# Performance work log

Hardware: AMD Instinct MI355X
Metric: run time of the kernel (lower is better)

## Reference

```python
import jax, jax.numpy as jnp
import numpy as np

D_MODEL = 2048
D_STATE = 128
D_CONV = 4
EXPAND = 2
HEADDIM = 64
NGROUPS = 1
D_INNER = EXPAND * D_MODEL            # 4096
NHEADS = D_INNER // HEADDIM           # 64
D_XBC = D_INNER + 2 * NGROUPS * D_STATE   # 4352
D_IN_PROJ = 2 * D_INNER + 2 * NGROUPS * D_STATE + NHEADS  # 8512
BLOCK_LEN = 64


def _segsum(x):
    # x: (..., T) -> (..., T, T) with segsum[i, j] = sum_{j < k <= i} x[k], -inf above diag
    T = x.shape[-1]
    xc = jnp.cumsum(x, axis=-1)
    seg = xc[..., :, None] - xc[..., None, :]
    mask = jnp.tril(jnp.ones((T, T), dtype=bool))
    return jnp.where(mask, seg, -jnp.inf)


def _ssd_scan(X, A, B, C, block_len):
    # X: (b, L, h, p), A: (b, L, h), B/C: (b, L, h, n)
    b, L, h, p = X.shape
    c = L // block_len
    X = X.reshape(b, c, block_len, h, p)
    A = A.reshape(b, c, block_len, h).transpose(0, 3, 1, 2)  # b h c l
    B = B.reshape(b, c, block_len, h, -1)
    C = C.reshape(b, c, block_len, h, -1)
    A_cumsum = jnp.cumsum(A, axis=-1)                         # b h c l
    Lmat = jnp.exp(_segsum(A))                                # b h c l l
    Y_diag = jnp.einsum('bclhn,bcshn,bhcls,bcshp->bclhp', C, B, Lmat, X)
    decay_states = jnp.exp(A_cumsum[:, :, :, -1:] - A_cumsum)  # b h c l
    states = jnp.einsum('bclhn,bhcl,bclhp->bchpn', B, decay_states, X)
    init = jnp.zeros_like(states[:, :1])
    states = jnp.concatenate([init, states], axis=1)          # b (c+1) h p n
    A_last = jnp.pad(A_cumsum[:, :, :, -1], ((0, 0), (0, 0), (1, 0)))  # b h (c+1)
    decay_chunk = jnp.exp(_segsum(A_last))                    # b h (c+1) (c+1)
    new_states = jnp.einsum('bhzc,bchpn->bzhpn', decay_chunk, states)
    states = new_states[:, 1:]                                # b c h p n
    state_decay_out = jnp.exp(A_cumsum)                       # b h c l
    Y_off = jnp.einsum('bclhn,bchpn,bhcl->bclhp', C, states, state_decay_out)
    return (Y_diag + Y_off).reshape(b, L, h, p)


def _forward(x, in_proj_w, conv_w, conv_b, A_log, D, dt_bias, norm_w, out_proj_w):
    Bsz, L, _ = x.shape
    proj = x @ in_proj_w.T                                    # (B, L, d_in_proj)
    z = proj[:, :, :D_INNER]
    xBC = proj[:, :, D_INNER:D_INNER + D_XBC]
    dt_raw = proj[:, :, D_INNER + D_XBC:]
    # depthwise causal conv1d (torch pads both sides then truncates to L == left pad only)
    xBC_t = xBC.transpose(0, 2, 1)                            # (B, C, L)
    conv = jax.lax.conv_general_dilated(
        xBC_t, conv_w, window_strides=(1,), padding=[(D_CONV - 1, 0)],
        feature_group_count=D_XBC, dimension_numbers=('NCH', 'OIH', 'NCH'))
    conv = conv + conv_b[None, :, None]
    xBC = jax.nn.silu(conv).transpose(0, 2, 1)                # (B, L, d_xBC)
    x_ssm = xBC[:, :, :D_INNER]
    B_param = xBC[:, :, D_INNER:D_INNER + NGROUPS * D_STATE]
    C_param = xBC[:, :, D_INNER + NGROUPS * D_STATE:]
    dt = jax.nn.softplus(dt_raw + dt_bias)                    # (B, L, nheads)
    A = -jnp.exp(A_log)                                       # (nheads,)
    x_heads = x_ssm.reshape(Bsz, L, NHEADS, HEADDIM)
    hpg = NHEADS // NGROUPS
    X = x_heads * dt[..., None]
    A_disc = dt * A[None, None, :]
    B_heads = jnp.repeat(B_param.reshape(Bsz, L, NGROUPS, D_STATE), hpg, axis=2)
    C_heads = jnp.repeat(C_param.reshape(Bsz, L, NGROUPS, D_STATE), hpg, axis=2)
    pad_len = (BLOCK_LEN - L % BLOCK_LEN) % BLOCK_LEN
    if pad_len > 0:
        X = jnp.pad(X, ((0, 0), (0, pad_len), (0, 0), (0, 0)))
        A_disc = jnp.pad(A_disc, ((0, 0), (0, pad_len), (0, 0)))
        B_heads = jnp.pad(B_heads, ((0, 0), (0, pad_len), (0, 0), (0, 0)))
        C_heads = jnp.pad(C_heads, ((0, 0), (0, pad_len), (0, 0), (0, 0)))
    Y = _ssd_scan(X, A_disc, B_heads, C_heads, BLOCK_LEN)[:, :L]
    Y = Y + x_heads * D[None, None, :, None]
    y = Y.reshape(Bsz, L, D_INNER)
    y = y * jax.nn.silu(z)
    rms = jnp.sqrt(jnp.mean(y * y, axis=-1, keepdims=True) + 1e-5)
    y = y / rms * norm_w
    return y @ out_proj_w.T


def setup_inputs() -> dict:
    key = jax.random.key(0)
    ks = jax.random.split(key, 8)
    x = jax.random.normal(ks[0], (2, 2048, D_MODEL), dtype=jnp.float32)
    in_proj_w = jax.random.normal(ks[1], (D_IN_PROJ, D_MODEL), dtype=jnp.float32) * 0.02
    conv_w = jax.random.normal(ks[2], (D_XBC, 1, D_CONV), dtype=jnp.float32) * 0.2
    conv_b = jnp.zeros((D_XBC,), dtype=jnp.float32)
    A_log = jnp.log(jnp.arange(1, NHEADS + 1, dtype=jnp.float32))
    D = jnp.ones((NHEADS,), dtype=jnp.float32)
    dt_bias = jax.random.normal(ks[3], (NHEADS,), dtype=jnp.float32) * 0.1
    norm_w = jnp.ones((D_INNER,), dtype=jnp.float32)
    out_proj_w = jax.random.normal(ks[4], (D_MODEL, D_INNER), dtype=jnp.float32) * 0.02
    return {"x": x, "in_proj_w": in_proj_w, "conv_w": conv_w, "conv_b": conv_b,
            "A_log": A_log, "D": D, "dt_bias": dt_bias, "norm_w": norm_w,
            "out_proj_w": out_proj_w}


def reference(x, in_proj_w, conv_w, conv_b, A_log, D, dt_bias, norm_w, out_proj_w):
    return _forward(x, in_proj_w, conv_w, conv_b, A_log, D, dt_bias, norm_w, out_proj_w)
```

## Files before the change

### kernel.cpp

```cpp
#include <hip/hip_runtime.h>
#include <cstddef>
#include <cstdint>

#define B_SZ    2
#define SEQ     2048
#define DMODEL  2048
#define DINNER  4096
#define DSTATE  128
#define NHEADS  64
#define HEADDIM 64
#define DXBC    4352
#define NPROJ   8448
#define CHUNK   64
#define NCHUNK  32
#define TOKENS  (B_SZ*SEQ)

typedef __attribute__((ext_vector_type(8))) short short8;
typedef __attribute__((ext_vector_type(4))) float floatx4;

__device__ inline float us2f(unsigned short u) {
  union { uint32_t i; float f; } c; c.i = ((uint32_t)u) << 16; return c.f;
}
__device__ inline unsigned short f2us(float f) {
  union { float f; uint32_t i; } c; c.f = f;
  uint32_t r = (c.i + 0x7fffu + ((c.i >> 16) & 1u)) >> 16;
  return (unsigned short)r;
}
__device__ inline float plo(uint32_t v) {
  union { uint32_t i; float f; } c; c.i = v << 16; return c.f;
}
__device__ inline float phi(uint32_t v) {
  union { uint32_t i; float f; } c; c.i = v & 0xffff0000u; return c.f;
}

__global__ __launch_bounds__(256) void cast_f32_bf16(
    const float* __restrict__ src, unsigned short* __restrict__ dst, int n) {
  int i = (blockIdx.x * 256 + threadIdx.x) * 4;
  if (i < n) {
    float4 v = *(const float4*)(src + i);
    ushort4 o;
    o.x = f2us(v.x); o.y = f2us(v.y); o.z = f2us(v.z); o.w = f2us(v.w);
    *(ushort4*)(dst + i) = o;
  }
}

template<int OUT_BF16>
__global__ __launch_bounds__(256, 2) void gemm_bt_p3(
    const unsigned short* __restrict__ A, const unsigned short* __restrict__ B,
    void* __restrict__ Cout, int M, int N, int K, int GM) {
  __shared__ __align__(16) unsigned short sT[3 * 12288];
  const int tid  = threadIdx.x;
  const int lane = tid & 63;
  const int wc   = tid >> 6;
  const int fr   = lane & 15;
  const int fq   = lane >> 4;

  const int nwg  = gridDim.x;
  int wgid = blockIdx.x;
  if ((nwg & 7) == 0) wgid = (wgid & 7) * (nwg >> 3) + (wgid >> 3);
  const int bm = (wgid % GM) * 128;
  const int bn = (wgid / GM) * 256;

  floatx4 acc[8][4];
  #pragma unroll
  for (int i = 0; i < 8; ++i)
    #pragma unroll
    for (int j = 0; j < 4; ++j) acc[i][j] = (floatx4){0.f, 0.f, 0.f, 0.f};

  auto stage = [&](int rb, int kb) {
    unsigned short* dst = (unsigned short*)sT + rb * 12288;
    #pragma unroll
    for (int q = 0; q < 6; ++q) {
      if (q < 2) {
        int i = q * 256 + tid;
        int row = i >> 2, slot = i & 3;
        const unsigned short* g =
            A + (size_t)(bm + row) * K + kb + 8 * (slot ^ ((row >> 1) & 3));
        __builtin_amdgcn_global_load_lds(
            (const __attribute__((address_space(1))) uint32_t*)g,
            (__attribute__((address_space(3))) uint32_t*)(dst + i * 8), 16, 0, 0);
      } else {
        int i = (q - 2) * 256 + tid;
        int row = i >> 2, slot = i & 3;
        const unsigned short* g =
            B + (size_t)(bn + row) * K + kb + 8 * (slot ^ ((row >> 1) & 3));
        __builtin_amdgcn_global_load_lds(
            (const __attribute__((address_space(1))) uint32_t*)g,
            (__attribute__((address_space(3))) uint32_t*)(dst + 4096 + i * 8), 16, 0, 0);
      }
    }
  };

  const int NH = K >> 5;
  stage(0, 0);
  stage(1, 32);
  asm volatile("s_waitcnt vmcnt(6)" ::: "memory");
  asm volatile("s_barrier" ::: "memory");

  int cb = 0, sb = 2;
  for (int h = 0; h < NH; ++h) {
    const unsigned short* buf = (const unsigned short*)sT + cb * 12288;
    if (h + 2 < NH) stage(sb, (h + 2) << 5);

    short8 af[8], bf[4];
    #pragma unroll
    for (int i = 0; i < 8; ++i) {
      int row = i * 16 + fr;
      af[i] = *(const short8*)(buf + row * 32 + 8 * (fq ^ ((row >> 1) & 3)));
    }
    #pragma unroll
    for (int j = 0; j < 4; ++j) {
      int row = wc * 64 + j * 16 + fr;
      bf[j] = *(const short8*)(buf + 4096 + row * 32 + 8 * (fq ^ ((row >> 1) & 3)));
    }
    __builtin_amdgcn_s_setprio(1);
    #pragma unroll
    for (int i = 0; i < 8; ++i)
      #pragma unroll
      for (int j = 0; j < 4; ++j)
        acc[i][j] = __builtin_amdgcn_mfma_f32_16x16x32_bf16(af[i], bf[j], acc[i][j], 0, 0, 0);
    __builtin_amdgcn_s_setprio(0);

    if (h < NH - 2) asm volatile("s_waitcnt vmcnt(6) lgkmcnt(0)" ::: "memory");
    else            asm volatile("s_waitcnt vmcnt(0) lgkmcnt(0)" ::: "memory");
    asm volatile("s_barrier" ::: "memory");
    cb = (cb == 2) ? 0 : cb + 1;
    sb = (sb == 2) ? 0 : sb + 1;
  }

  #pragma unroll
  for (int i = 0; i < 8; ++i) {
    #pragma unroll
    for (int j = 0; j < 4; ++j) {
      int col = bn + wc * 64 + j * 16 + fr;
      #pragma unroll
      for (int r = 0; r < 4; ++r) {
        int row = bm + i * 16 + fq * 4 + r;
        if (OUT_BF16)
          ((unsigned short*)Cout)[(size_t)row * N + col] = f2us(acc[i][j][r]);
        else
          ((float*)Cout)[(size_t)row * N + col] = acc[i][j][r];
      }
    }
  }
}

__device__ inline void loadA4(const float* p, float* d) {
  float4 v = *(const float4*)p; d[0]=v.x; d[1]=v.y; d[2]=v.z; d[3]=v.w;
}
__device__ inline void loadA4(const unsigned short* p, float* d) {
  ushort4 v = *(const ushort4*)p;
  d[0]=us2f(v.x); d[1]=us2f(v.y); d[2]=us2f(v.z); d[3]=us2f(v.w);
}
__device__ inline void store8(float* C, size_t off, const float* v) {
  *(float4*)(C + off)     = make_float4(v[0], v[1], v[2], v[3]);
  *(float4*)(C + off + 4) = make_float4(v[4], v[5], v[6], v[7]);
}
__device__ inline void store8(unsigned short* C, size_t off, const float* v) {
  ushort4 a; a.x=f2us(v[0]); a.y=f2us(v[1]); a.z=f2us(v[2]); a.w=f2us(v[3]);
  ushort4 b; b.x=f2us(v[4]); b.y=f2us(v[5]); b.z=f2us(v[6]); b.w=f2us(v[7]);
  *(ushort4*)(C + off) = a; *(ushort4*)(C + off + 4) = b;
}

template<typename AT, typename OT>
__global__ __launch_bounds__(256) void gemm_nt(
    const AT* __restrict__ A, const float* __restrict__ Bw,
    OT* __restrict__ C, int M, int N, int K) {
  __shared__ float As[16][128+4];
  __shared__ float Bs[16][128+4];
  const int bm = blockIdx.y * 128;
  const int bn = blockIdx.x * 128;
  const int tid = threadIdx.x;
  const int tx = tid & 15, ty = tid >> 4;

  float acc[8][8];
  #pragma unroll
  for (int i = 0; i < 8; ++i)
    #pragma unroll
    for (int j = 0; j < 8; ++j) acc[i][j] = 0.f;

  for (int k0 = 0; k0 < K; k0 += 16) {
    #pragma unroll
    for (int r = 0; r < 2; ++r) {
      int i = tid + r * 256;
      int m  = i >> 2;
      int kv = (i & 3) << 2;
      float va[4];
      loadA4(A + (size_t)(bm + m) * K + k0 + kv, va);
      As[kv+0][m] = va[0]; As[kv+1][m] = va[1]; As[kv+2][m] = va[2]; As[kv+3][m] = va[3];
      float vb[4] = {0.f, 0.f, 0.f, 0.f};
      if (bn + m < N) loadA4(Bw + (size_t)(bn + m) * K + k0 + kv, vb);
      Bs[kv+0][m] = vb[0]; Bs[kv+1][m] = vb[1]; Bs[kv+2][m] = vb[2]; Bs[kv+3][m] = vb[3];
    }
    __syncthreads();
    #pragma unroll
    for (int kk = 0; kk < 16; ++kk) {
      float ra[8], rb[8];
      *(float4*)&ra[0] = *(const float4*)&As[kk][ty*8];
      *(float4*)&ra[4] = *(const float4*)&As[kk][ty*8+4];
      *(float4*)&rb[0] = *(const float4*)&Bs[kk][tx*8];
      *(float4*)&rb[4] = *(const float4*)&Bs[kk][tx*8+4];
      #pragma unroll
      for (int i = 0; i < 8; ++i)
        #pragma unroll
        for (int j = 0; j < 8; ++j) acc[i][j] += ra[i] * rb[j];
    }
    __syncthreads();
  }
  #pragma unroll
  for (int i = 0; i < 8; ++i) {
    int m  = bm + ty*8 + i;
    int n0 = bn + tx*8;
    if (n0 < N) store8(C, (size_t)m * N + n0, &acc[i][0]);
  }
}

__global__ __launch_bounds__(256) void dt_gemm(
    const float* __restrict__ x, const float* __restrict__ W,
    float* __restrict__ dtr) {
  __shared__ float sX[32][64];
  __shared__ float sW[32][64];
  const int tid = threadIdx.x;
  const int t0 = blockIdx.x * 64;
  const int tx = tid & 15;
  const int ty = tid >> 4;
  const float* Wdt = W + (size_t)NPROJ * DMODEL;

  float acc[4][4];
  #pragma unroll
  for (int i = 0; i < 4; ++i)
    #pragma unroll
    for (int j = 0; j < 4; ++j) acc[i][j] = 0.f;

  const int r  = tid >> 3;
  const int kq = (tid & 7) * 4;

  for (int k0 = 0; k0 < DMODEL; k0 += 32) {
    __syncthreads();
    #pragma unroll
    for (int rr = 0; rr < 2; ++rr) {
      int t = r + rr * 32;
      float4 v = *(const float4*)(x + (size_t)(t0 + t) * DMODEL + k0 + kq);
      sX[kq+0][t] = v.x; sX[kq+1][t] = v.y; sX[kq+2][t] = v.z; sX[kq+3][t] = v.w;
    }
    #pragma unroll
    for (int rr = 0; rr < 2; ++rr) {
      int hh = r + rr * 32;
      float4 v = *(const float4*)(Wdt + (size_t)hh * DMODEL + k0 + kq);
      sW[kq+0][hh] = v.x; sW[kq+1][hh] = v.y; sW[kq+2][hh] = v.z; sW[kq+3][hh] = v.w;
    }
    __syncthreads();
    #pragma unroll
    for (int kk = 0; kk < 32; ++kk) {
      float4 ra = *(const float4*)&sX[kk][ty*4];
      float4 rb = *(const float4*)&sW[kk][tx*4];
      float a[4] = {ra.x, ra.y, ra.z, ra.w};
      float b[4] = {rb.x, rb.y, rb.z, rb.w};
      #pragma unroll
      for (int i = 0; i < 4; ++i)
        #pragma unroll
        for (int j = 0; j < 4; ++j)
          acc[i][j] += a[i] * b[j];
    }
  }
  #pragma unroll
  for (int i = 0; i < 4; ++i) {
    float4 o = make_float4(acc[i][0], acc[i][1], acc[i][2], acc[i][3]);
    *(float4*)(dtr + (size_t)(t0 + ty*4 + i) * NHEADS + tx*4) = o;
  }
}

__global__ __launch_bounds__(256) void bc_conv_g(
    const unsigned short* __restrict__ proj, const float* __restrict__ cw,
    const float* __restrict__ cb, unsigned short* __restrict__ bcact,
    float* __restrict__ gbuf) {
  const int c = blockIdx.x & 31;
  const int b = blockIdx.x >> 5;
  const int tid = threadIdx.x;
  const int t0 = b * SEQ + c * CHUNK;
  __shared__ unsigned short sB[64*130];
  __shared__ unsigned short sC[64*130];
  for (int i = tid; i < 64*256; i += 256) {
    int s = i >> 8, ch = i & 255;
    int cx = 4096 + ch;
    int lb = c * CHUNK + s;
    float acc = cb[cx];
    #pragma unroll
    for (int j = 0; j < 4; ++j) {
      int ll = lb - 3 + j;
      if (ll >= 0)
        acc += cw[cx*4 + j] * us2f(proj[(size_t)(b*SEQ + ll) * NPROJ + DINNER + cx]);
    }
    float v = acc / (1.f + expf(-acc));
    unsigned short uv = f2us(v);
    if (ch < 128) sB[s*130 + ch] = uv;
    else          sC[s*130 + (ch - 128)] = uv;
    bcact[(size_t)(t0 + s) * 256 + ch] = uv;
  }
  __syncthreads();
  const int l = tid >> 2, q = tid & 3;
  float g[16];
  #pragma unroll
  for (int j = 0; j < 16; ++j) g[j] = 0.f;
  const uint32_t* Cu = (const uint32_t*)&sC[l * 130];
  for (int u = 0; u < 64; ++u) {
    uint32_t cv = Cu[u];
    float c0 = plo(cv), c1 = phi(cv);
    #pragma unroll
    for (int j = 0; j < 16; ++j) {
      uint32_t bv = ((const uint32_t*)&sB[(q*16 + j) * 130])[u];
      g[j] += c0 * plo(bv) + c1 * phi(bv);
    }
  }
  float* gr = gbuf + ((size_t)(b*NCHUNK + c)) * 4096 + l*64 + q*16;
  #pragma unroll
  for (int j = 0; j < 16; ++j) gr[j] = g[j];
}

__global__ __launch_bounds__(256, 4) void ssd_phase_a2_mfma(
    const unsigned short* __restrict__ proj, const unsigned short* __restrict__ bcact,
    const float* __restrict__ dtr, const float* __restrict__ cw,
    const float* __restrict__ cb, const float* __restrict__ A_log,
    const float* __restrict__ dt_bias, const float* __restrict__ gbuf,
    const float* __restrict__ Dv,
    unsigned short* __restrict__ cs, float* __restrict__ acs,
    unsigned short* __restrict__ yscan) {
  const int h = blockIdx.x & 63;
  const int c = (blockIdx.x >> 6) & 31;
  const int b = blockIdx.x >> 11;
  const int tid = threadIdx.x;
  const int t0 = b * SEQ + c * CHUNK;
  const int lane = tid & 63, wave = tid >> 6;
  const int fr = lane & 15, fq = lane >> 4;

  __shared__ __align__(16) unsigned short sBt[128*72];
  __shared__ __align__(16) unsigned short sXh[64*72];
  __shared__ __align__(16) unsigned short sW[64*72];
  __shared__ float sdt[64], sAc[64], sdecay[64];

  const float Ah = -expf(A_log[h]);
  if (tid < 64) {
    float raw = dtr[(size_t)(t0 + tid) * NHEADS + h] + dt_bias[h];
    float dt = (raw > 20.f) ? raw : log1pf(expf(raw));
    sdt[tid] = dt;
    float v = dt * Ah;
    #pragma unroll
    for (int off = 1; off < 64; off <<= 1) {
      float o = __shfl_up(v, off, 64);
      if (tid >= off) v += o;
    }
    sAc[tid] = v;
    float alast = __shfl(v, 63, 64);
    sdecay[tid] = expf(alast - v);
    acs[((size_t)((b*NHEADS + h)*NCHUNK + c))*64 + tid] = v;
  }
  __syncthreads();
  for (int i = tid; i < 64*128; i += 256) {
    int s = i >> 7, n = i & 127;
    float v = us2f(bcact[(size_t)(t0 + s) * 256 + n]) * sdt[s] * sdecay[s];
    sBt[n*72 + s] = f2us(v);
  }
  for (int i = tid; i < 64*64; i += 256) {
    int s = i >> 6, p = i & 63;
    int cx = h * HEADDIM + p;
    int lb = c * CHUNK + s;
    float acc = cb[cx];
    #pragma unroll
    for (int j = 0; j < 4; ++j) {
      int ll = lb - 3 + j;
      if (ll >= 0)
        acc += cw[cx*4 + j] * us2f(proj[(size_t)(b*SEQ + ll) * NPROJ + DINNER + cx]);
    }
    float xh = acc / (1.f + expf(-acc));
    sXh[p*72 + s] = f2us(xh);
  }
  {
    const float* gr = gbuf + ((size_t)(b*NCHUNK + c)) * 4096;
    for (int i = tid; i < 4096; i += 256) {
      int l = i >> 6, s = i & 63;
      float w = (s <= l) ? gr[i] * expf(sAc[l] - sAc[s]) * sdt[s] : 0.f;
      sW[l*72 + s] = f2us(w);
    }
  }
  __syncthreads();

  floatx4 accy[4];
  #pragma unroll
  for (int j = 0; j < 4; ++j) accy[j] = (floatx4){0.f, 0.f, 0.f, 0.f};
  #pragma unroll
  for (int k0 = 0; k0 < 64; k0 += 32) {
    short8 af = *(const short8*)(sW + (wave*16 + fr)*72 + k0 + fq*8);
    #pragma unroll
    for (int j = 0; j < 4; ++j) {
      short8 bf = *(const short8*)(sXh + (j*16 + fr)*72 + k0 + fq*8);
      accy[j] = __builtin_amdgcn_mfma_f32_16x16x32_bf16(af, bf, accy[j], 0, 0, 0);
    }
  }
  const float Dh = Dv[h];
  #pragma unroll
  for (int j = 0; j < 4; ++j) {
    int p = j*16 + fr;
    #pragma unroll
    for (int r = 0; r < 4; ++r) {
      int l = wave*16 + fq*4 + r;
      float yd = accy[j][r] + us2f(sXh[p*72 + l]) * Dh;
      yscan[(size_t)(t0 + l) * DINNER + h*HEADDIM + p] = f2us(yd);
    }
  }
  floatx4 accs[8];
  #pragma unroll
  for (int j = 0; j < 8; ++j) accs[j] = (floatx4){0.f, 0.f, 0.f, 0.f};
  #pragma unroll
  for (int k0 = 0; k0 < 64; k0 += 32) {
    short8 af = *(const short8*)(sXh + (wave*16 + fr)*72 + k0 + fq*8);
    #pragma unroll
    for (int j = 0; j < 8; ++j) {
      short8 bf = *(const short8*)(sBt + (j*16 + fr)*72 + k0 + fq*8);
      accs[j] = __builtin_amdgcn_mfma_f32_16x16x32_bf16(af, bf, accs[j], 0, 0, 0);
    }
  }
  const size_t csb = ((size_t)((b*NHEADS + h)*NCHUNK + c)) * (HEADDIM*DSTATE);
  #pragma unroll
  for (int j = 0; j < 8; ++j) {
    int n = j*16 + fr;
    #pragma unroll
    for (int r = 0; r < 4; ++r) {
      int p = wave*16 + fq*4 + r;
      cs[csb + p*128 + n] = f2us(accs[j][r]);
    }
  }
}

__global__ __launch_bounds__(256) void ssd_scan_states(
    unsigned short* __restrict__ cs, const float* __restrict__ acs) {
  int idx = blockIdx.x * 256 + threadIdx.x;
  int e  = idx & 8191;
  int bh = idx >> 13;
  float S = 0.f;
  for (int c = 0; c < NCHUNK; ++c) {
    float al = acs[((size_t)bh*NCHUNK + c)*64 + 63];
    size_t o = ((size_t)bh*NCHUNK + c)*(HEADDIM*DSTATE) + e;
    S = S * expf(al) + us2f(cs[o]);
    cs[o] = f2us(S);
  }
}

__global__ __launch_bounds__(256, 4) void ssd_phase_c_mfma(
    const unsigned short* __restrict__ bcact, const unsigned short* __restrict__ cs,
    const float* __restrict__ acs, unsigned short* __restrict__ yscan) {
  const int h = blockIdx.x & 63;
  const int c = (blockIdx.x >> 6) & 31;
  const int b = blockIdx.x >> 11;
  const int tid = threadIdx.x;
  const int t0 = b * SEQ + c * CHUNK;
  const int lane = tid & 63, wave = tid >> 6;
  const int fr = lane & 15, fq = lane >> 4;

  __shared__ __align__(16) unsigned short sC[64*136];
  __shared__ __align__(16) unsigned short sS[64*136];
  __shared__ float seAc[64];

  const size_t csb = ((size_t)((b*NHEADS + h)*NCHUNK + c)) * (HEADDIM*DSTATE);
  for (int i = tid; i < 8192; i += 256) {
    int p = i >> 7, n = i & 127;
    sS[p*136 + n] = cs[csb + i];
  }
  for (int i = tid; i < 8192; i += 256) {
    int l = i >> 7, n = i & 127;
    sC[l*136 + n] = bcact[(size_t)(t0 + l) * 256 + 128 + n];
  }
  if (tid < 64) seAc[tid] = expf(acs[((size_t)((b*NHEADS + h)*NCHUNK + c))*64 + tid]);
  __syncthreads();

  floatx4 acc[4];
  #pragma unroll
  for (int j = 0; j < 4; ++j) acc[j] = (floatx4){0.f, 0.f, 0.f, 0.f};
  #pragma unroll
  for (int k0 = 0; k0 < 128; k0 += 32) {
    short8 af = *(const short8*)(sC + (wave*16 + fr)*136 + k0 + fq*8);
    #pragma unroll
    for (int j = 0; j < 4; ++j) {
      short8 bf = *(const short8*)(sS + (j*16 + fr)*136 + k0 + fq*8);
      acc[j] = __builtin_amdgcn_mfma_f32_16x16x32_bf16(af, bf, acc[j], 0, 0, 0);
    }
  }
  #pragma unroll
  for (int j = 0; j < 4; ++j) {
    int p = j*16 + fr;
    #pragma unroll
    for (int r = 0; r < 4; ++r) {
      int l = wave*16 + fq*4 + r;
      size_t yi = (size_t)(t0 + l) * DINNER + h*HEADDIM + p;
      yscan[yi] = f2us(us2f(yscan[yi]) + acc[j][r] * seAc[l]);
    }
  }
}

__global__ __launch_bounds__(256) void gate_rmsnorm2(
    const unsigned short* __restrict__ proj, const float* __restrict__ norm_w,
    unsigned short* __restrict__ yscan) {
  const int t = blockIdx.x;
  const int tid = threadIdx.x;
  __shared__ float ybuf[DINNER];
  __shared__ float wpart[4];
  __shared__ float sinv;
  float ss = 0.f;
  for (int i = tid; i < DINNER; i += 256) {
    float zv = us2f(proj[(size_t)t * NPROJ + i]);
    float yv = us2f(yscan[(size_t)t * DINNER + i]) * (zv / (1.f + expf(-zv)));
    ybuf[i] = yv;
    ss += yv * yv;
  }
  #pragma unroll
  for (int off = 32; off > 0; off >>= 1) ss += __shfl_down(ss, off, 64);
  if ((tid & 63) == 0) wpart[tid >> 6] = ss;
  __syncthreads();
  if (tid == 0) {
    float tot = wpart[0] + wpart[1] + wpart[2] + wpart[3];
    sinv = 1.f / sqrtf(tot / (float)DINNER + 1e-5f);
  }
  __syncthreads();
  float inv = sinv;
  for (int i = tid; i < DINNER; i += 256)
    yscan[(size_t)t * DINNER + i] = f2us(ybuf[i] * inv * norm_w[i]);
}

__global__ __launch_bounds__(512) void ssd_fused(
    const unsigned short* __restrict__ proj, const float* __restrict__ dtr,
    const float* __restrict__ cw, const float* __restrict__ cb,
    const float* __restrict__ A_log, const float* __restrict__ dt_bias,
    unsigned short* __restrict__ yscan) {
  const int h = blockIdx.x & 63;
  const int b = blockIdx.x >> 6;
  const int tid = threadIdx.x;

  __shared__ unsigned short sB[64*130];
  __shared__ unsigned short sC[64*130];
  __shared__ unsigned short sX[64*66];
  __shared__ float sW[64*65];
  __shared__ float sdt[64], sAc[64], sdecay[64], seAc[64];

  const float Ah = -expf(A_log[h]);
  const float dbias = dt_bias[h];

  float S[16];
  #pragma unroll
  for (int j = 0; j < 16; ++j) S[j] = 0.f;

  const int lG  = tid >> 3;
  const int oc  = tid & 7;

  for (int c = 0; c < NCHUNK; ++c) {
    const int t0 = b * SEQ + c * CHUNK;
    __syncthreads();
    if (tid < 64) {
      float raw = dtr[(size_t)(t0 + tid) * NHEADS + h] + dbias;
      sdt[tid] = (raw > 20.f) ? raw : log1pf(expf(raw));
    }
    for (int i = tid; i < 64*256; i += 512) {
      int s = i >> 8, ch = i & 255;
      int cx = 4096 + ch;
      int lb = c * CHUNK + s;
      float acc = cb[cx];
      #pragma unroll
      for (int j = 0; j < 4; ++j) {
        int ll = lb - 3 + j;
        if (ll >= 0)
          acc += cw[cx*4 + j] * us2f(proj[(size_t)(b*SEQ + ll) * NPROJ + DINNER + cx]);
      }
      float v = acc / (1.f + expf(-acc));
      if (ch < 128) sB[s*130 + ch] = f2us(v);
      else          sC[s*130 + (ch - 128)] = f2us(v);
    }
    __syncthreads();
    if (tid == 0) {
      float run = 0.f;
      for (int s = 0; s < CHUNK; ++s) { run += sdt[s] * Ah; sAc[s] = run; }
    }
    __syncthreads();
    if (tid < 64) {
      float last = sAc[63];
      sdecay[tid] = expf(last - sAc[tid]);
      seAc[tid]   = expf(sAc[tid]);
    }
    for (int i = tid; i < 64*64; i += 512) {
      int s = i >> 6, p = i & 63;
      int cx = h * HEADDIM + p;
      int lb = c * CHUNK + s;
      float acc = cb[cx];
      #pragma unroll
      for (int j = 0; j < 4; ++j) {
        int ll = lb - 3 + j;
        if (ll >= 0)
          acc += cw[cx*4 + j] * us2f(proj[(size_t)(b*SEQ + ll) * NPROJ + DINNER + cx]);
      }
      float v = acc / (1.f + expf(-acc));
      sX[s*66 + p] = f2us(v * sdt[s]);
    }
    __syncthreads();

    float g[8];
    #pragma unroll
    for (int j = 0; j < 8; ++j) g[j] = 0.f;
    {
      const uint32_t* Cu = (const uint32_t*)&sC[lG * 130];
      for (int u = 0; u < 64; ++u) {
        uint32_t cv = Cu[u];
        float c0 = plo(cv), c1 = phi(cv);
        #pragma unroll
        for (int j = 0; j < 8; ++j) {
          uint32_t bv = ((const uint32_t*)&sB[(oc*8 + j) * 130])[u];
          g[j] += c0 * plo(bv) + c1 * phi(bv);
        }
      }
    }
    {
      float acl = sAc[lG];
      #pragma unroll
      for (int j = 0; j < 8; ++j) {
        int s = oc*8 + j;
        sW[lG*65 + s] = (s <= lG) ? g[j] * expf(acl - sAc[s]) : 0.f;
      }
    }
    {
      float elast = expf(sAc[63]);
      #pragma unroll
      for (int j = 0; j < 16; ++j) S[j] *= elast;
      for (int s = 0; s < CHUNK; ++s) {
        float w = sdecay[s] * us2f(sX[s*66 + lG]);
        const uint32_t* Bu = (const uint32_t*)&sB[s*130 + oc*16];
        #pragma unroll
        for (int ju = 0; ju < 8; ++ju) {
          uint32_t bv = Bu[ju];
          S[2*ju]   += plo(bv) * w;
          S[2*ju+1] += phi(bv) * w;
        }
      }
    }
    __syncthreads();
    #pragma unroll
    for (int j = 0; j < 16; ++j) sB[lG*130 + oc*16 + j] = f2us(S[j]);
    __syncthreads();
    for (int o = tid; o < CHUNK*HEADDIM; o += 512) {
      int l = o >> 6, p = o & 63;
      float yd = 0.f;
      for (int s = 0; s <= l; ++s)
        yd += sW[l*65 + s] * us2f(sX[s*66 + p]);
      float yo = 0.f;
      const uint32_t* Cu = (const uint32_t*)&sC[l * 130];
      const uint32_t* Su = (const uint32_t*)&sB[p * 130];
      for (int u = 0; u < 64; ++u) {
        uint32_t cv = Cu[u], sv = Su[u];
        yo += plo(cv) * plo(sv) + phi(cv) * phi(sv);
      }
      float y = yd + yo * seAc[l];
      yscan[(size_t)(t0 + l) * DINNER + h * HEADDIM + p] = f2us(y);
    }
  }
}

__global__ __launch_bounds__(256) void gate_rmsnorm_dskip(
    const unsigned short* __restrict__ proj, const float* __restrict__ cw,
    const float* __restrict__ cb, const float* __restrict__ Dv,
    const float* __restrict__ norm_w, unsigned short* __restrict__ yscan) {
  const int t = blockIdx.x;
  const int tid = threadIdx.x;
  const int b = t >> 11, lb = t & 2047;
  __shared__ float ybuf[DINNER];
  __shared__ float wpart[4];
  __shared__ float sinv;
  float ss = 0.f;
  for (int i = tid; i < DINNER; i += 256) {
    float zv = us2f(proj[(size_t)t * NPROJ + i]);
    float acc = cb[i];
    #pragma unroll
    for (int j = 0; j < 4; ++j) {
      int ll = lb - 3 + j;
      if (ll >= 0)
        acc += cw[i*4 + j] * us2f(proj[(size_t)(b*SEQ + ll) * NPROJ + DINNER + i]);
    }
    float xh = acc / (1.f + expf(-acc));
    float yv = us2f(yscan[(size_t)t * DINNER + i]) + xh * Dv[i >> 6];
    yv = yv * (zv / (1.f + expf(-zv)));
    ybuf[i] = yv;
    ss += yv * yv;
  }
  #pragma unroll
  for (int off = 32; off > 0; off >>= 1) ss += __shfl_down(ss, off, 64);
  if ((tid & 63) == 0) wpart[tid >> 6] = ss;
  __syncthreads();
  if (tid == 0) {
    float tot = wpart[0] + wpart[1] + wpart[2] + wpart[3];
    sinv = 1.f / sqrtf(tot / (float)DINNER + 1e-5f);
  }
  __syncthreads();
  float inv = sinv;
  for (int i = tid; i < DINNER; i += 256)
    yscan[(size_t)t * DINNER + i] = f2us(ybuf[i] * inv * norm_w[i]);
}

extern "C" void kernel_launch(void* const* d_in, const int* in_sizes, int n_in,
                              void* d_out, int out_size, void* d_ws, size_t ws_size,
                              hipStream_t stream) {
  const float* x          = (const float*)d_in[0];
  const float* in_proj_w  = (const float*)d_in[1];
  const float* conv_w     = (const float*)d_in[2];
  const float* conv_b     = (const float*)d_in[3];
  const float* A_log      = (const float*)d_in[4];
  const float* Dv         = (const float*)d_in[5];
  const float* dt_bias    = (const float*)d_in[6];
  const float* norm_w     = (const float*)d_in[7];
  const float* out_proj_w = (const float*)d_in[8];
  float* out = (float*)d_out;

  unsigned short* proj  = (unsigned short*)d_ws;
  float*          dtr   = (float*)(proj + (size_t)TOKENS * NPROJ);
  unsigned short* yscan = (unsigned short*)(dtr + (size_t)TOKENS * NHEADS);
  unsigned short* cs    = yscan + (size_t)TOKENS * DINNER;
  float*          acs   = (float*)(cs + (size_t)B_SZ*NHEADS*NCHUNK*HEADDIM*DSTATE);
  unsigned short* bcact = (unsigned short*)(acs + (size_t)B_SZ*NHEADS*NCHUNK*64);
  float*          gbuf  = (float*)(bcact + (size_t)TOKENS*256);
  const size_t NEEDED = (size_t)((char*)(gbuf + (size_t)B_SZ*NCHUNK*4096) - (char*)d_ws);

  unsigned short* xb  = cs;
  unsigned short* wib = xb + (size_t)TOKENS * DMODEL;
  unsigned short* wob = proj;

  if (ws_size >= NEEDED) {
    cast_f32_bf16<<<(TOKENS*DMODEL)/1024, 256, 0, stream>>>(x, xb, TOKENS*DMODEL);
    cast_f32_bf16<<<((size_t)NPROJ*DMODEL)/1024, 256, 0, stream>>>(in_proj_w, wib, NPROJ*DMODEL);
    {
      int nwg = (TOKENS/128) * (NPROJ/256);
      gemm_bt_p3<1><<<nwg, 256, 0, stream>>>(xb, wib, proj, TOKENS, NPROJ, DMODEL, TOKENS/128);
    }
    dt_gemm<<<TOKENS/64, 256, 0, stream>>>(x, in_proj_w, dtr);
    bc_conv_g<<<B_SZ*NCHUNK, 256, 0, stream>>>(proj, conv_w, conv_b, bcact, gbuf);
    ssd_phase_a2_mfma<<<B_SZ*NCHUNK*NHEADS, 256, 0, stream>>>(
        proj, bcact, dtr, conv_w, conv_b, A_log, dt_bias, gbuf, Dv, cs, acs, yscan);
    ssd_scan_states<<<(B_SZ*NHEADS*HEADDIM*DSTATE)/256, 256, 0, stream>>>(cs, acs);
    ssd_phase_c_mfma<<<B_SZ*NCHUNK*NHEADS, 256, 0, stream>>>(bcact, cs, acs, yscan);
    gate_rmsnorm2<<<TOKENS, 256, 0, stream>>>(proj, norm_w, yscan);
    cast_f32_bf16<<<((size_t)DMODEL*DINNER)/1024, 256, 0, stream>>>(out_proj_w, wob, DMODEL*DINNER);
    {
      int nwg = (TOKENS/128) * (DMODEL/256);
      gemm_bt_p3<0><<<nwg, 256, 0, stream>>>(yscan, wob, out, TOKENS, DMODEL, DINNER, TOKENS/128);
    }
  } else {
    {
      dim3 grid(NPROJ/128, TOKENS/128);
      gemm_nt<float, unsigned short><<<grid, 256, 0, stream>>>(
          x, in_proj_w, proj, TOKENS, NPROJ, DMODEL);
    }
    dt_gemm<<<TOKENS/64, 256, 0, stream>>>(x, in_proj_w, dtr);
    ssd_fused<<<B_SZ*NHEADS, 512, 0, stream>>>(proj, dtr, conv_w, conv_b,
                                               A_log, dt_bias, yscan);
    gate_rmsnorm_dskip<<<TOKENS, 256, 0, stream>>>(proj, conv_w, conv_b, Dv, norm_w, yscan);
    {
      dim3 grid(DMODEL/128, TOKENS/128);
      gemm_nt<unsigned short, float><<<grid, 256, 0, stream>>>(
          yscan, out_proj_w, out, TOKENS, DMODEL, DINNER);
    }
  }
}
```

Baseline: 796.0 us.

## Split GEMM k-step into two half-phases interleaving LDS reads, prefetch, and MFMA

Each k-iteration of the bf16 GEMM main loop is split into two phases. Each phase loads half the A fragments from LDS, issues half of the next-stage global-to-LDS prefetch, and then runs 16 MFMAs, with barriers between phases. The aim is to spread the memory issue across the MFMA work, ping-pong style, so that load issue and LDS reads overlap with tensor compute. In exchange it adds extra barriers per iteration, and the vmcnt accounting now spans the split stage.

Result: no change. 807.2 us (+1.4%).

```diff
diff --git a/kernel.cpp b/kernel.cpp
--- a/kernel.cpp
+++ b/kernel.cpp
@@ -67,10 +67,11 @@
     #pragma unroll
     for (int j = 0; j < 4; ++j) acc[i][j] = (floatx4){0.f, 0.f, 0.f, 0.f};
 
-  auto stage = [&](int rb, int kb) {
+  auto stage3 = [&](int rb, int kb, int half) {
     unsigned short* dst = (unsigned short*)sT + rb * 12288;
     #pragma unroll
-    for (int q = 0; q < 6; ++q) {
+    for (int qq = 0; qq < 3; ++qq) {
+      int q = half * 3 + qq;
       if (q < 2) {
         int i = q * 256 + tid;
         int row = i >> 2, slot = i & 3;
@@ -92,19 +93,20 @@
   };
 
   const int NH = K >> 5;
-  stage(0, 0);
-  stage(1, 32);
+  stage3(0, 0, 0); stage3(0, 0, 1);
+  stage3(1, 32, 0); stage3(1, 32, 1);
   asm volatile("s_waitcnt vmcnt(6)" ::: "memory");
   asm volatile("s_barrier" ::: "memory");
 
   int cb = 0, sb = 2;
   for (int h = 0; h < NH; ++h) {
     const unsigned short* buf = (const unsigned short*)sT + cb * 12288;
-    if (h + 2 < NH) stage(sb, (h + 2) << 5);
+    const int k2 = (h + 2) << 5;
+    const bool pre = (h + 2 < NH);
 
     short8 af[8], bf[4];
     #pragma unroll
-    for (int i = 0; i < 8; ++i) {
+    for (int i = 0; i < 4; ++i) {
       int row = i * 16 + fr;
       af[i] = *(const short8*)(buf + row * 32 + 8 * (fq ^ ((row >> 1) & 3)));
     }
@@ -113,17 +115,37 @@
       int row = wc * 64 + j * 16 + fr;
       bf[j] = *(const short8*)(buf + 4096 + row * 32 + 8 * (fq ^ ((row >> 1) & 3)));
     }
+    if (pre) stage3(sb, k2, 0);
+    asm volatile("s_barrier" ::: "memory");
+    asm volatile("s_waitcnt lgkmcnt(0)" ::: "memory");
     __builtin_amdgcn_s_setprio(1);
     #pragma unroll
-    for (int i = 0; i < 8; ++i)
+    for (int i = 0; i < 4; ++i)
       #pragma unroll
       for (int j = 0; j < 4; ++j)
         acc[i][j] = __builtin_amdgcn_mfma_f32_16x16x32_bf16(af[i], bf[j], acc[i][j], 0, 0, 0);
     __builtin_amdgcn_s_setprio(0);
-
-    if (h < NH - 2) asm volatile("s_waitcnt vmcnt(6) lgkmcnt(0)" ::: "memory");
-    else            asm volatile("s_waitcnt vmcnt(0) lgkmcnt(0)" ::: "memory");
     asm volatile("s_barrier" ::: "memory");
+
+    #pragma unroll
+    for (int i = 4; i < 8; ++i) {
+      int row = i * 16 + fr;
+      af[i] = *(const short8*)(buf + row * 32 + 8 * (fq ^ ((row >> 1) & 3)));
+    }
+    if (pre) stage3(sb, k2, 1);
+    if (h < NH - 2) asm volatile("s_waitcnt vmcnt(6)" ::: "memory");
+    else            asm volatile("s_waitcnt vmcnt(0)" ::: "memory");
+    asm volatile("s_barrier" ::: "memory");
+    asm volatile("s_waitcnt lgkmcnt(0)" ::: "memory");
+    __builtin_amdgcn_s_setprio(1);
+    #pragma unroll
+    for (int i = 4; i < 8; ++i)
+      #pragma unroll
+      for (int j = 0; j < 4; ++j)
+        acc[i][j] = __builtin_amdgcn_mfma_f32_16x16x32_bf16(af[i], bf[j], acc[i][j], 0, 0, 0);
+    __builtin_amdgcn_s_setprio(0);
+    asm volatile("s_barrier" ::: "memory");
+
     cb = (cb == 2) ? 0 : cb + 1;
     sb = (sb == 2) ? 0 : sb + 1;
   }
```
